# Performance work log

Measured on AMD Instinct MI355X. Metric: run time of the kernel, lower is better.

The kernel has to match this reference:

```python
import jax, jax.numpy as jnp
import numpy as np

# Emformer hyper-parameters (init_kwargs)
SEG = 128   # segment_length
RC = 32     # right_context_length
LC = 64     # left_context_length
MEM = 4     # max_memory_length (>0 -> 9 column groups)
N = 64      # num_segments
U = N * SEG # utterance_length (divisible by SEG => static row counts)
NUM_COLS = 9


def setup_inputs() -> dict:
    # Standard Emformer column masks: attend to own memory slot, own right-context
    # block and own (left-context-extended) segment.
    rc_q = np.array([0, 1, 0, 0, 1, 0, 0, 1, 0], dtype=bool)
    s = np.array([0, 1, 0, 0, 0, 0, 0, 1, 0], dtype=bool)
    return {
        "indices": jnp.arange(N - 1, dtype=jnp.int32)[:, None],                # (N-1, 1)
        "utt_lengths": jnp.full((N, 1), U, dtype=jnp.int32),                   # (N, 1)
        "rc_q_cols_mask_tile": jnp.asarray(np.tile(rc_q, (N - 1, 1))),         # (N-1, 9) bool
        "last_idx": jnp.full((1, 1), N - 1, dtype=jnp.int32),                  # (1, 1)
        "last_utt_lengths": jnp.full((1,), U, dtype=jnp.int32),                # (1,)
        "last_rc_q_cols_mask": jnp.asarray(rc_q[:, None]),                     # (9, 1) bool
        "s_cols_mask_tile": jnp.asarray(np.tile(s, (N - 1, 1))),               # (N-1, 9) bool
        "last_s_cols_mask": jnp.asarray(s[:, None]),                           # (9, 1) bool
    }


def _col_widths(seg_idx, num_segments, utt_len):
    """Per-segment widths of the 9 column groups. seg_idx: (N,) int32 -> (N, 9)."""
    mem_start = jnp.maximum(0, seg_idx - MEM)
    rc_start = seg_idx * RC
    seg_start = jnp.maximum(0, seg_idx * SEG - LC)
    seg_end = jnp.minimum(utt_len, (seg_idx + 1) * SEG)
    rcv = jnp.full_like(seg_idx, RC)
    return jnp.stack([
        mem_start, seg_idx - mem_start, (num_segments - 1) - seg_idx,   # memory blocks
        rc_start, rcv, RC * num_segments - (rc_start + RC),             # right-context blocks
        seg_start, seg_end - seg_start, utt_len - seg_end,              # utterance blocks
    ], axis=1)


def reference(indices, utt_lengths, rc_q_cols_mask_tile, last_idx,
              last_utt_lengths, last_rc_q_cols_mask,
              s_cols_mask_tile, last_s_cols_mask):
    # Stack all N segments (map_fn segments + the explicit last segment).
    seg_idx = jnp.concatenate([indices[:, 0], last_idx[0]]).astype(jnp.int32)          # (N,)
    rc_masks = jnp.concatenate([rc_q_cols_mask_tile,
                                jnp.transpose(last_rc_q_cols_mask)], axis=0)          # (N, 9) bool
    s_masks = jnp.concatenate([s_cols_mask_tile,
                               jnp.transpose(last_s_cols_mask)], axis=0)              # (N, 9) bool

    W = (N - 1) + RC * N + U                         # total mask width (constant per row)
    widths = _col_widths(seg_idx, N, U)              # (N, 9)
    cum_end = jnp.cumsum(widths, axis=1)             # (N, 9), last column == W

    # For each segment row, map each column j to its column-group index:
    # grp[i, j] = #{k : cum_end[i, k] <= j}  (zero-width groups are skipped correctly).
    j = jnp.arange(W, dtype=jnp.int32)
    grp = jnp.sum(j[None, :, None] >= cum_end[:, None, :], axis=-1)  # (N, W) in [0, 8]

    rc_vals = jnp.take_along_axis(rc_masks, grp, axis=1)  # (N, W) bool: 1-blocks vs 0-blocks
    s_vals = jnp.take_along_axis(s_masks, grp, axis=1)    # (N, W) bool

    # rc block: RC identical rows per segment; query block: SEG rows per segment
    # (U == N * SEG, so min(SEG, U - i*SEG) == SEG for every segment);
    # summary block: 1 row per segment.
    rc_block = jnp.repeat(rc_vals, RC, axis=0)   # (RC*N, W)
    q_block = jnp.repeat(rc_vals, SEG, axis=0)   # (U, W)
    full = jnp.concatenate([rc_block, q_block, s_vals], axis=0)  # (RC*N + U + N, W) bool

    # Original: attention_mask = (1 - mask) > 0, i.e. True where attention is disallowed.
    return jnp.logical_not(full)
```

## Files before the change

### kernel.cpp

```cpp
#include <hip/hip_runtime.h>

namespace {
constexpr int SEG  = 128;
constexpr int RCL  = 32;
constexpr int LC   = 64;
constexpr int MEM  = 4;
constexpr int NSEG = 64;
constexpr int U    = NSEG * SEG;
constexpr int W    = (NSEG - 1) + RCL * NSEG + U;
constexpr int RC_ROWS  = RCL * NSEG;
constexpr int SUM_BASE = RC_ROWS + U;
constexpr int UTT_BASE = (NSEG - 1) + RCL * NSEG;

constexpr int COL_TILES  = 4;
constexpr int CPT        = 2576;
constexpr int ROW_GROUPS = 8;
constexpr int KMAX       = 11;
}

__global__ __launch_bounds__(256) void emformer_mask_kernel(int* __restrict__ out) {
    const int tid = (int)threadIdx.x;
    const int rg  = (int)blockIdx.x;
    const int ct  = (int)blockIdx.y;
    const int i   = (int)blockIdx.z;

    const int colbase = ct * CPT;
    const int ncols   = min(CPT, W - colbase);

    const int a0 = max(i - MEM, 0);
    const int a1 = i;
    const int b0 = (NSEG - 1) + RCL * i;
    const int d0 = UTT_BASE + max(SEG * i - LC, 0);
    const int d1 = UTT_BASE + SEG * (i + 1);

    int vq[KMAX], vs[KMAX];
#pragma unroll
    for (int k = 0; k < KMAX; ++k) {
        const int c = colbase + tid + (k << 8);
        const bool inA = (unsigned)(c - a0) < (unsigned)(a1 - a0);
        const bool inB = (unsigned)(c - b0) < (unsigned)RCL;
        const bool inD = (unsigned)(c - d0) < (unsigned)(d1 - d0);
        vq[k] = (inA | inB | inD) ? 0 : 1;
        vs[k] = (inA | inD) ? 0 : 1;
    }

    const bool has_tail = tid < (ncols - (KMAX - 1) * 256);

    int* __restrict__ p = out + (size_t)colbase + tid;

    {
        const int r0 = RCL * i + rg * 4;
        for (int rr = 0; rr < 4; ++rr) {
            int* __restrict__ rowp = p + (size_t)(r0 + rr) * W;
#pragma unroll
            for (int k = 0; k < KMAX - 1; ++k) rowp[k << 8] = vq[k];
            if (has_tail) rowp[(KMAX - 1) << 8] = vq[KMAX - 1];
        }
    }
    {
        const int r0 = RC_ROWS + SEG * i + rg * 16;
        for (int rr = 0; rr < 16; ++rr) {
            int* __restrict__ rowp = p + (size_t)(r0 + rr) * W;
#pragma unroll
            for (int k = 0; k < KMAX - 1; ++k) rowp[k << 8] = vq[k];
            if (has_tail) rowp[(KMAX - 1) << 8] = vq[KMAX - 1];
        }
    }
    if (rg == 0) {
        int* __restrict__ rowp = p + (size_t)(SUM_BASE + i) * W;
#pragma unroll
        for (int k = 0; k < KMAX - 1; ++k) rowp[k << 8] = vs[k];
        if (has_tail) rowp[(KMAX - 1) << 8] = vs[KMAX - 1];
    }
}

extern "C" void kernel_launch(void* const* d_in, const int* in_sizes, int n_in,
                              void* d_out, int out_size, void* d_ws, size_t ws_size,
                              hipStream_t stream) {
    (void)d_in; (void)in_sizes; (void)n_in; (void)d_ws; (void)ws_size; (void)out_size;
    emformer_mask_kernel<<<dim3(ROW_GROUPS, COL_TILES, NSEG), dim3(256), 0, stream>>>(
        (int*)d_out);
}
```

Baseline: 483.1 us.

## Stage per-segment mask row in LDS and emit 16-byte vector stores over flattened ranges

Each block now builds the segment's query and summary mask rows once as bytes in shared memory. It then walks a flattened, evenly split range of the segment's output (RC rows, query rows, summary row) and writes 128-bit int4 stores, unpacking four bytes per store from LDS. The aim is to replace scalar 4-byte stores with wide stores and to balance work evenly across blocks. This adds a modulo per thread, unaligned-word reads from LDS and a smaller grid (24x64 blocks).

```diff
diff --git a/kernel.cpp b/kernel.cpp
--- a/kernel.cpp
+++ b/kernel.cpp
@@ -9,23 +9,64 @@
 constexpr int U    = NSEG * SEG;
 constexpr int W    = (NSEG - 1) + RCL * NSEG + U;
 constexpr int RC_ROWS  = RCL * NSEG;
-constexpr int SUM_BASE = RC_ROWS + U;
 constexpr int UTT_BASE = (NSEG - 1) + RCL * NSEG;
+constexpr int W_PAD = 10312;
 
-constexpr int COL_TILES  = 4;
-constexpr int CPT        = 2576;
-constexpr int ROW_GROUPS = 8;
-constexpr int KMAX       = 11;
+constexpr unsigned C0 = 32u * W;
+constexpr unsigned C1 = 160u * W;
+constexpr unsigned C2 = 161u * W;
+constexpr int P = 24;
+constexpr unsigned PER = (C2 + P - 1) / P;
+}
+
+typedef int i32x4 __attribute__((ext_vector_type(4)));
+
+__device__ __forceinline__ void do_piece(const unsigned char* __restrict__ img,
+                                         int* __restrict__ out,
+                                         unsigned f0, unsigned f1,
+                                         unsigned rbaseW, int tid) {
+    const unsigned fa = (f0 + 3u) & ~3u;
+    const unsigned fe = f1 & ~3u;
+    if (fa >= fe) {
+        for (unsigned f = f0 + (unsigned)tid; f < f1; f += 256u)
+            out[f] = (int)img[(f - rbaseW) % (unsigned)W];
+        return;
+    }
+    if ((unsigned)tid < fa - f0) {
+        unsigned f = f0 + (unsigned)tid;
+        out[f] = (int)img[(f - rbaseW) % (unsigned)W];
+    }
+    if ((unsigned)tid < f1 - fe) {
+        unsigned f = fe + (unsigned)tid;
+        out[f] = (int)img[(f - rbaseW) % (unsigned)W];
+    }
+    const unsigned qa = fa >> 2, qe = fe >> 2;
+    unsigned c = (fa + 4u * (unsigned)tid - rbaseW) % (unsigned)W;
+    const unsigned* __restrict__ im32 = (const unsigned*)img;
+    i32x4* __restrict__ o = (i32x4*)out + qa + (unsigned)tid;
+    for (unsigned q = qa + (unsigned)tid; q < qe; q += 256u, o += 256) {
+        const unsigned wc = c >> 2;
+        const unsigned sh = (c & 3u) * 8u;
+        const unsigned w0 = im32[wc];
+        const unsigned w1 = im32[wc + 1];
+        const unsigned packed =
+            (unsigned)(((((unsigned long long)w1) << 32) | w0) >> sh);
+        i32x4 v;
+        v.x = (int)(packed & 0xffu);
+        v.y = (int)((packed >> 8) & 0xffu);
+        v.z = (int)((packed >> 16) & 0xffu);
+        v.w = (int)(packed >> 24);
+        *o = v;
+        c += 1024u;
+        if (c >= (unsigned)W) c -= (unsigned)W;
+    }
 }
 
 __global__ __launch_bounds__(256) void emformer_mask_kernel(int* __restrict__ out) {
+    __shared__ __align__(16) unsigned char s_img[2][W_PAD];
     const int tid = (int)threadIdx.x;
-    const int rg  = (int)blockIdx.x;
-    const int ct  = (int)blockIdx.y;
-    const int i   = (int)blockIdx.z;
-
-    const int colbase = ct * CPT;
-    const int ncols   = min(CPT, W - colbase);
+    const int b   = (int)blockIdx.x;
+    const int i   = (int)blockIdx.y;
 
     const int a0 = max(i - MEM, 0);
     const int a1 = i;
@@ -33,44 +74,35 @@
     const int d0 = UTT_BASE + max(SEG * i - LC, 0);
     const int d1 = UTT_BASE + SEG * (i + 1);
 
-    int vq[KMAX], vs[KMAX];
-#pragma unroll
-    for (int k = 0; k < KMAX; ++k) {
-        const int c = colbase + tid + (k << 8);
+    for (int c = tid; c < W; c += 256) {
         const bool inA = (unsigned)(c - a0) < (unsigned)(a1 - a0);
         const bool inB = (unsigned)(c - b0) < (unsigned)RCL;
         const bool inD = (unsigned)(c - d0) < (unsigned)(d1 - d0);
-        vq[k] = (inA | inB | inD) ? 0 : 1;
-        vs[k] = (inA | inD) ? 0 : 1;
+        s_img[0][c] = (inA | inB | inD) ? 0 : 1;
+        s_img[1][c] = (inA | inD) ? 0 : 1;
     }
+    if (tid < 8) {
+        s_img[0][W + tid] = s_img[0][tid];
+        s_img[1][W + tid] = s_img[1][tid];
+    }
+    __syncthreads();
 
-    const bool has_tail = tid < (ncols - (KMAX - 1) * 256);
+    const unsigned v0 = (unsigned)b * PER;
+    const unsigned v1 = min(v0 + PER, C2);
 
-    int* __restrict__ p = out + (size_t)colbase + tid;
-
-    {
-        const int r0 = RCL * i + rg * 4;
-        for (int rr = 0; rr < 4; ++rr) {
-            int* __restrict__ rowp = p + (size_t)(r0 + rr) * W;
-#pragma unroll
-            for (int k = 0; k < KMAX - 1; ++k) rowp[k << 8] = vq[k];
-            if (has_tail) rowp[(KMAX - 1) << 8] = vq[KMAX - 1];
-        }
+    if (v0 < C0) {
+        const unsigned rbW = (unsigned)(RCL * i) * (unsigned)W;
+        do_piece(s_img[0], out, rbW + v0, rbW + min(v1, C0), rbW, tid);
     }
-    {
-        const int r0 = RC_ROWS + SEG * i + rg * 16;
-        for (int rr = 0; rr < 16; ++rr) {
-            int* __restrict__ rowp = p + (size_t)(r0 + rr) * W;
-#pragma unroll
-            for (int k = 0; k < KMAX - 1; ++k) rowp[k << 8] = vq[k];
-            if (has_tail) rowp[(KMAX - 1) << 8] = vq[KMAX - 1];
-        }
+    if (v1 > C0 && v0 < C1) {
+        const unsigned s = max(v0, C0), e = min(v1, C1);
+        const unsigned rbW = (unsigned)(RC_ROWS + SEG * i) * (unsigned)W;
+        do_piece(s_img[0], out, rbW + (s - C0), rbW + (e - C0), rbW, tid);
     }
-    if (rg == 0) {
-        int* __restrict__ rowp = p + (size_t)(SUM_BASE + i) * W;
-#pragma unroll
-        for (int k = 0; k < KMAX - 1; ++k) rowp[k << 8] = vs[k];
-        if (has_tail) rowp[(KMAX - 1) << 8] = vs[KMAX - 1];
+    if (v1 > C1) {
+        const unsigned s = max(v0, C1);
+        const unsigned rbW = (unsigned)(RC_ROWS + U + i) * (unsigned)W;
+        do_piece(s_img[1], out, rbW + (s - C1), rbW + (v1 - C1), rbW, tid);
     }
 }
 
@@ -78,6 +110,5 @@
                               void* d_out, int out_size, void* d_ws, size_t ws_size,
                               hipStream_t stream) {
     (void)d_in; (void)in_sizes; (void)n_in; (void)d_ws; (void)ws_size; (void)out_size;
-    emformer_mask_kernel<<<dim3(ROW_GROUPS, COL_TILES, NSEG), dim3(256), 0, stream>>>(
-        (int*)d_out);
+    emformer_mask_kernel<<<dim3(P, NSEG), dim3(256), 0, stream>>>((int*)d_out);
 }
```

After: 438.4 us. 1.1x faster.
